# Optimization experiments

Hardware: AMD Instinct MI355X
Metric: run time of the kernel (lower is better)

The kernel has to match this reference:

```python
import jax, jax.numpy as jnp
import numpy as np

D = 256          # common_dim = specific_dim
NH = 8           # num_heads
HD = D // NH     # head_dim = 32
B, S = 16, 1024
EPS = 1e-5


def _mha(q, k, v, wq, bq, wk, bk, wv, bv, wo, bo):
    # q,k,v: [B, S, D]; weights stored [in, out] so y = x @ w + b
    b_, _, _ = q.shape

    def proj(x, w, b):
        return (x @ w + b).reshape(b_, -1, NH, HD).transpose(0, 2, 1, 3)  # [B,H,S,hd]

    Q, K, V = proj(q, wq, bq), proj(k, wk, bk), proj(v, wv, bv)
    scores = jnp.einsum('bhqd,bhkd->bhqk', Q, K) / (float(HD) ** 0.5)
    attn = jax.nn.softmax(scores, axis=-1)
    out = jnp.einsum('bhqk,bhkd->bhqd', attn, V)
    out = out.transpose(0, 2, 1, 3).reshape(b_, -1, D)
    return out @ wo + bo


def _ln(x, g, b):
    mu = jnp.mean(x, axis=-1, keepdims=True)
    var = jnp.var(x, axis=-1, keepdims=True)
    return (x - mu) * jax.lax.rsqrt(var + EPS) * g + b


def setup_inputs() -> dict:
    key = jax.random.key(0)
    ks = iter(jax.random.split(key, 32))
    rn = lambda *shape: jax.random.normal(next(ks), shape, dtype=jnp.float32)
    w = lambda i, o: rn(i, o) * 0.05
    inp = {
        'img_common': rn(B, S, D),
        'txt_common': rn(B, S, D),
        'img_specific': rn(B, D),
        'txt_specific': rn(B, D),
    }
    for pfx in ('i2t', 't2i'):
        for nm in ('q', 'k', 'v', 'o'):
            inp[f'{pfx}_w{nm}'] = w(D, D)
            inp[f'{pfx}_b{nm}'] = jnp.zeros((D,), jnp.float32)
    inp['ln_img_g'] = jnp.ones((D,), jnp.float32)
    inp['ln_img_b'] = jnp.zeros((D,), jnp.float32)
    inp['ln_txt_g'] = jnp.ones((D,), jnp.float32)
    inp['ln_txt_b'] = jnp.zeros((D,), jnp.float32)
    inp['enh_w'] = w(2 * D, D)
    inp['enh_b'] = jnp.zeros((D,), jnp.float32)
    inp['inc_w'] = w(2 * D, D)
    inp['inc_b'] = jnp.zeros((D,), jnp.float32)
    return inp


def reference(img_common, txt_common, img_specific, txt_specific,
              i2t_wq, i2t_bq, i2t_wk, i2t_bk, i2t_wv, i2t_bv, i2t_wo, i2t_bo,
              t2i_wq, t2i_bq, t2i_wk, t2i_bk, t2i_wv, t2i_bv, t2i_wo, t2i_bo,
              ln_img_g, ln_img_b, ln_txt_g, ln_txt_b,
              enh_w, enh_b, inc_w, inc_b):
    att_i2t = _mha(img_common, txt_common, txt_common,
                   i2t_wq, i2t_bq, i2t_wk, i2t_bk, i2t_wv, i2t_bv, i2t_wo, i2t_bo)
    img_query = _ln(att_i2t + img_common, ln_img_g, ln_img_b)
    att_t2i = _mha(txt_common, img_common, img_common,
                   t2i_wq, t2i_bq, t2i_wk, t2i_bk, t2i_wv, t2i_bv, t2i_wo, t2i_bo)
    txt_query = _ln(att_t2i + txt_common, ln_txt_g, ln_txt_b)
    combined = jnp.concatenate((img_query, txt_query), axis=-1)  # [B,S,2D]
    enhancement = combined @ enh_w + enh_b                        # [B,S,D]
    inc = jnp.concatenate((img_specific - txt_specific,
                           img_specific * txt_specific), axis=1)  # [B,2D]
    inconsistency = inc @ inc_w + inc_b                           # [B,D]
    return (enhancement, inconsistency, img_specific, txt_specific)
```

## Files before the change

kernel.cpp:

```cpp
#include <hip/hip_runtime.h>
#include <stdint.h>

typedef unsigned int u32;
typedef unsigned short u16;
typedef __attribute__((ext_vector_type(8))) short bf16x8;
typedef __attribute__((ext_vector_type(4))) float f32x4;

#define BUF_ELEMS (16384 * 256)

__device__ __forceinline__ float bflo(u32 u) { return __uint_as_float(u << 16); }
__device__ __forceinline__ float bfhi(u32 u) { return __uint_as_float(u & 0xffff0000u); }
__device__ __forceinline__ u16 f2bf(float f) {
    u32 u = __float_as_uint(f);
    return (u16)((u + 0x7fffu + ((u >> 16) & 1u)) >> 16);
}
__device__ __forceinline__ u32 pkhi(float lo, float hi) {
    return __builtin_amdgcn_perm(__float_as_uint(hi), __float_as_uint(lo), 0x07060302u);
}

struct WT {
    const float* src[9];
    u16* dst[9];
    const float* bs[6];
    float* bA;
    float* bB;
    const float* img_sp;
    const float* txt_sp;
    const float* incw;
    const float* incb;
    float* out_inc;
    float* out_img;
    float* out_txt;
};

__global__ __launch_bounds__(256)
void wtrans_kernel(WT wt)
{
    __shared__ float T[64][65];
    const int bid = blockIdx.x, t = threadIdx.x;
    if (bid == 160) {
        wt.bA[t]       = wt.bs[0][t];
        wt.bA[256 + t] = wt.bs[1][t];
        wt.bA[512 + t] = wt.bs[2][t];
        wt.bB[t]       = wt.bs[3][t];
        wt.bB[256 + t] = wt.bs[4][t];
        wt.bB[512 + t] = wt.bs[5][t];
        return;
    }
    if (bid > 160) {
        float* iv = &T[0][0];
        const int b = bid - 161, n = t;
        float a = wt.img_sp[b * 256 + n];
        float x = wt.txt_sp[b * 256 + n];
        iv[n] = a - x;
        iv[256 + n] = a * x;
        __syncthreads();
        float acc = wt.incb[n];
        for (int k = 0; k < 512; k++) acc += iv[k] * wt.incw[k * 256 + n];
        wt.out_inc[b * 256 + n] = acc;
        wt.out_img[b * 256 + n] = a;
        wt.out_txt[b * 256 + n] = x;
        return;
    }
    int m, sub;
    if (bid < 128) { m = bid >> 4; sub = bid & 15; }
    else           { m = 8;        sub = bid - 128; }
    const int K = (m == 8) ? 512 : 256;
    const int kt = (m == 8) ? (sub & 7) : (sub & 3);
    const int nt = (m == 8) ? (sub >> 3) : (sub >> 2);
    const int k0 = kt * 64, n0 = nt * 64;
    const float* src = wt.src[m];
    u16* dst = wt.dst[m];

    const int kk = t >> 2, nn = (t & 3) * 16;
    #pragma unroll
    for (int j = 0; j < 16; j += 4) {
        float4 v = *(const float4*)(src + (size_t)(k0 + kk) * 256 + n0 + nn + j);
        T[kk][nn + j + 0] = v.x; T[kk][nn + j + 1] = v.y;
        T[kk][nn + j + 2] = v.z; T[kk][nn + j + 3] = v.w;
    }
    __syncthreads();
    const int nn2 = t >> 2, kc = (t & 3) * 16;
    #pragma unroll
    for (int j = 0; j < 16; j++)
        dst[(size_t)(n0 + nn2) * K + k0 + kc + j] = f2bf(T[kc + j][nn2]);
}

template<int MODE>
__global__ __launch_bounds__(256)
void gemm_mfma(const float* __restrict__ Af0, const float* __restrict__ Af1,
               const u16* __restrict__ Ab0, const u16* __restrict__ Ab1,
               const u16* __restrict__ Wt0, const u16* __restrict__ Wt1,
               const float* __restrict__ bias0, const float* __restrict__ bias1,
               void* __restrict__ o0, void* __restrict__ o1, void* __restrict__ o2,
               void* __restrict__ o3, void* __restrict__ o4, void* __restrict__ o5)
{
    __shared__ u16 As[128][72];
    __shared__ u16 Bs[128][72];
    const int tid = threadIdx.x;
    const int wave = tid >> 6, lane = tid & 63;
    const int L = lane & 15, Qd = lane >> 4;
    int m_idx, n_idx;
    if (MODE == 0)      { m_idx = blockIdx.x & 255; n_idx = blockIdx.x >> 8; }
    else if (MODE == 1) { m_idx = blockIdx.x & 255; n_idx = blockIdx.x >> 8; }
    else                { m_idx = blockIdx.x & 127; n_idx = blockIdx.x >> 7; }
    const bool msel = (MODE != 2) && (m_idx >= 128 * (MODE == 0 ? 1 : 1) && MODE == 0
                       ? (m_idx >= 128) : (MODE == 1 && m_idx >= 128));
    const bool ms = (MODE == 0 || MODE == 1) ? (m_idx >= 128) : false;
    const int lm0 = (MODE == 2) ? m_idx * 128 : (m_idx & 127) * 128;
    const int n0 = n_idx * 128;
    const u16* Wt = ms ? Wt1 : Wt0;
    const float* bias = ms ? bias1 : bias0;
    const int wr = wave & 1, wc = wave >> 1;
    const int sr = tid >> 1, sh = (tid & 1) * 32;
    const int KS = (MODE == 2) ? 512 : 256;
    (void)msel;

    f32x4 acc[4][4] = {};

    for (int kt = 0; kt < KS; kt += 64) {
        if (MODE == 0) {
            const float* Af = ms ? Af1 : Af0;
            const float* Ap = Af + (size_t)(lm0 + sr) * 256 + kt + sh;
            uint4 pk[2];
            #pragma unroll
            for (int half = 0; half < 2; half++) {
                float4 f0 = *(const float4*)(Ap + half * 16);
                float4 f1 = *(const float4*)(Ap + half * 16 + 4);
                float4 f2 = *(const float4*)(Ap + half * 16 + 8);
                float4 f3 = *(const float4*)(Ap + half * 16 + 12);
                pk[half].x = pkhi(f0.x, f0.y);
                pk[half].y = pkhi(f0.z, f0.w);
                pk[half].z = pkhi(f1.x, f1.y);
                pk[half].w = pkhi(f1.z, f1.w);
                uint4 q;
                q.x = pkhi(f2.x, f2.y); q.y = pkhi(f2.z, f2.w);
                q.z = pkhi(f3.x, f3.y); q.w = pkhi(f3.z, f3.w);
                *(uint4*)&As[sr][sh + half * 16 + 8] = q;
            }
            *(uint4*)&As[sr][sh + 0] = pk[0];
            *(uint4*)&As[sr][sh + 16] = pk[1];
        } else {
            const u16* Abase;
            int lkt = kt;
            if (MODE == 2) { Abase = (kt < 256) ? Ab0 : Ab1; lkt = kt & 255; }
            else           { Abase = ms ? Ab1 : Ab0; }
            const u16* Ap = Abase + (size_t)(lm0 + sr) * 256 + lkt + sh;
            uint4 a0 = *(const uint4*)(Ap + 0);
            uint4 a1 = *(const uint4*)(Ap + 8);
            uint4 a2 = *(const uint4*)(Ap + 16);
            uint4 a3 = *(const uint4*)(Ap + 24);
            *(uint4*)&As[sr][sh + 0]  = a0;
            *(uint4*)&As[sr][sh + 8]  = a1;
            *(uint4*)&As[sr][sh + 16] = a2;
            *(uint4*)&As[sr][sh + 24] = a3;
        }
        {
            const u16* Bp = Wt + (size_t)(n0 + sr) * KS + kt + sh;
            uint4 w0 = *(const uint4*)(Bp + 0);
            uint4 w1 = *(const uint4*)(Bp + 8);
            uint4 w2 = *(const uint4*)(Bp + 16);
            uint4 w3 = *(const uint4*)(Bp + 24);
            *(uint4*)&Bs[sr][sh + 0]  = w0;
            *(uint4*)&Bs[sr][sh + 8]  = w1;
            *(uint4*)&Bs[sr][sh + 16] = w2;
            *(uint4*)&Bs[sr][sh + 24] = w3;
        }
        __syncthreads();
        #pragma unroll
        for (int kh = 0; kh < 64; kh += 32) {
            bf16x8 af[4], bf[4];
            #pragma unroll
            for (int mt = 0; mt < 4; mt++)
                af[mt] = *(const bf16x8*)&As[wr * 64 + mt * 16 + L][kh + Qd * 8];
            #pragma unroll
            for (int nt = 0; nt < 4; nt++)
                bf[nt] = *(const bf16x8*)&Bs[wc * 64 + nt * 16 + L][kh + Qd * 8];
            #pragma unroll
            for (int mt = 0; mt < 4; mt++)
                #pragma unroll
                for (int nt = 0; nt < 4; nt++)
                    acc[mt][nt] = __builtin_amdgcn_mfma_f32_16x16x32_bf16(
                        af[mt], bf[nt], acc[mt][nt], 0, 0, 0);
        }
        __syncthreads();
    }

    float bvals[4];
    #pragma unroll
    for (int nt = 0; nt < 4; nt++)
        bvals[nt] = bias[n0 + wc * 64 + nt * 16 + L];

    const float qsc = (MODE == 0 && n_idx < 2)
                      ? (0.17677669529663687f * 1.4426950408889634f) : 1.0f;

    void* outp;
    int colb;
    if (MODE == 0) {
        const int g = n_idx >> 1;
        if (!ms) outp = (g == 0) ? o0 : ((g == 1) ? o1 : o2);
        else     outp = (g == 0) ? o3 : ((g == 1) ? o4 : o5);
        colb = (n_idx & 1) * 128 + wc * 64;
    } else if (MODE == 1) {
        outp = ms ? o1 : o0;
        colb = n0 + wc * 64;
    } else {
        outp = o0;
        colb = n0 + wc * 64;
    }
    #pragma unroll
    for (int mt = 0; mt < 4; mt++) {
        #pragma unroll
        for (int r = 0; r < 4; r++) {
            const size_t row = (size_t)(lm0 + wr * 64 + mt * 16 + Qd * 4 + r) * 256;
            #pragma unroll
            for (int nt = 0; nt < 4; nt++) {
                const int col = colb + nt * 16 + L;
                float v = (acc[mt][nt][r] + bvals[nt]) * qsc;
                if (MODE == 2) ((float*)outp)[row + col] = v;
                else           ((u16*)outp)[row + col] = f2bf(v);
            }
        }
    }
}

__global__ __launch_bounds__(256, 4)
void attn_mfma(const u16* __restrict__ Q0, const u16* __restrict__ K0,
               const u16* __restrict__ V0, u16* __restrict__ O0,
               const u16* __restrict__ Q1, const u16* __restrict__ K1,
               const u16* __restrict__ V1, u16* __restrict__ O1)
{
    __shared__ u16 Ks[128][40];
    __shared__ u16 Vt[32][136];
    __shared__ u16 Ps[4][16][136];
    const int tid = threadIdx.x;
    const int wave = tid >> 6, lane = tid & 63;
    const int L = lane & 15, Qd = lane >> 4;
    const int bid = blockIdx.x;
    const int qt = bid >> 8;
    const int kv = bid & 255;
    const int set = kv >> 7;
    const int b = (kv >> 3) & 15;
    const int h = kv & 7;
    const u16* Q = set ? Q1 : Q0;
    const u16* K = set ? K1 : K0;
    const u16* V = set ? V1 : V0;
    u16* O = set ? O1 : O0;
    const int rowbase = b * 1024;
    const int qbase = rowbase + qt * 128;

    bf16x8 qfrag[2];
    #pragma unroll
    for (int qs = 0; qs < 2; qs++)
        qfrag[qs] = *(const bf16x8*)(Q + (size_t)(qbase + qs * 64 + wave * 16 + L) * 256
                                       + h * 32 + Qd * 8);

    const short oneb = (short)0x3F80;
    const bf16x8 ones = {oneb, oneb, oneb, oneb, oneb, oneb, oneb, oneb};

    f32x4 oacc[2][2] = {};
    f32x4 oaccL[2] = {};

    const int sr = tid >> 1;
    const int scol = (tid & 1) * 16;
    const int vcol = (sr & 15) * 8 + (sr >> 4);

    for (int t = 0; t < 8; t++) {
        const size_t kvbase = (size_t)(rowbase + t * 128 + sr) * 256 + h * 32 + scol;
        uint4 k1 = *(const uint4*)(K + kvbase);
        uint4 k2 = *(const uint4*)(K + kvbase + 8);
        uint4 v1 = *(const uint4*)(V + kvbase);
        uint4 v2 = *(const uint4*)(V + kvbase + 8);
        *(uint4*)&Ks[sr][scol]     = k1;
        *(uint4*)&Ks[sr][scol + 8] = k2;
        union { uint4 u4[2]; u16 us[16]; } vv;
        vv.u4[0] = v1; vv.u4[1] = v2;
        #pragma unroll
        for (int j = 0; j < 16; j++) Vt[scol + j][vcol] = vv.us[j];
        __syncthreads();

        bf16x8 kf[8];
        #pragma unroll
        for (int ct = 0; ct < 8; ct++)
            kf[ct] = *(const bf16x8*)&Ks[ct * 16 + L][Qd * 8];

        #pragma unroll
        for (int qs = 0; qs < 2; qs++) {
            const f32x4 z = {0.f, 0.f, 0.f, 0.f};
            f32x4 sacc[8];
            #pragma unroll
            for (int ct = 0; ct < 8; ct++)
                sacc[ct] = __builtin_amdgcn_mfma_f32_16x16x32_bf16(qfrag[qs], kf[ct], z, 0, 0, 0);
            #pragma unroll
            for (int r = 0; r < 4; r++) {
                float p[8];
                #pragma unroll
                for (int ct = 0; ct < 8; ct++) p[ct] = exp2f(sacc[ct][r]);
                uint4 pk;
                pk.x = pkhi(p[0], p[1]);
                pk.y = pkhi(p[2], p[3]);
                pk.z = pkhi(p[4], p[5]);
                pk.w = pkhi(p[6], p[7]);
                *(uint4*)&Ps[wave][Qd * 4 + r][L * 8] = pk;
            }
            #pragma unroll
            for (int kc = 0; kc < 4; kc++) {
                bf16x8 pfrag = *(const bf16x8*)&Ps[wave][L][kc * 32 + Qd * 8];
                bf16x8 vf0 = *(const bf16x8*)&Vt[L][kc * 32 + Qd * 8];
                bf16x8 vf1 = *(const bf16x8*)&Vt[16 + L][kc * 32 + Qd * 8];
                oacc[qs][0] = __builtin_amdgcn_mfma_f32_16x16x32_bf16(pfrag, vf0, oacc[qs][0], 0, 0, 0);
                oacc[qs][1] = __builtin_amdgcn_mfma_f32_16x16x32_bf16(pfrag, vf1, oacc[qs][1], 0, 0, 0);
                oaccL[qs]   = __builtin_amdgcn_mfma_f32_16x16x32_bf16(pfrag, ones, oaccL[qs], 0, 0, 0);
            }
        }
        __syncthreads();
    }

    #pragma unroll
    for (int qs = 0; qs < 2; qs++) {
        #pragma unroll
        for (int r = 0; r < 4; r++) {
            float inv = 1.f / oaccL[qs][r];
            const size_t orow = (size_t)(qbase + qs * 64 + wave * 16 + Qd * 4 + r) * 256 + h * 32;
            O[orow + L]      = f2bf(oacc[qs][0][r] * inv);
            O[orow + 16 + L] = f2bf(oacc[qs][1][r] * inv);
        }
    }
}

__global__ __launch_bounds__(256)
void ln_res_kernel(const u16* __restrict__ P0, const u16* __restrict__ P1,
                   const float* __restrict__ R0, const float* __restrict__ R1,
                   const float* __restrict__ g0, const float* __restrict__ be0,
                   const float* __restrict__ g1, const float* __restrict__ be1,
                   u16* __restrict__ out0, u16* __restrict__ out1)
{
    const int lane = threadIdx.x & 63;
    int row = blockIdx.x * 4 + (threadIdx.x >> 6);
    const bool sel = row >= 16384;
    const u16* P = sel ? P1 : P0;
    const float* R = sel ? R1 : R0;
    const float* g = sel ? g1 : g0;
    const float* be = sel ? be1 : be0;
    u16* out = sel ? out1 : out0;
    if (sel) row -= 16384;
    const int col = lane * 4;
    uint2 pv = *(const uint2*)(P + (size_t)row * 256 + col);
    float4 rv = *(const float4*)(R + (size_t)row * 256 + col);
    float x0 = bflo(pv.x) + rv.x;
    float x1 = bfhi(pv.x) + rv.y;
    float x2 = bflo(pv.y) + rv.z;
    float x3 = bfhi(pv.y) + rv.w;
    float s = x0 + x1 + x2 + x3;
    float s2 = x0*x0 + x1*x1 + x2*x2 + x3*x3;
    #pragma unroll
    for (int off = 32; off > 0; off >>= 1) {
        s  += __shfl_xor(s, off);
        s2 += __shfl_xor(s2, off);
    }
    float mean = s * 0.00390625f;
    float var = fmaxf(s2 * 0.00390625f - mean * mean, 0.f);
    float rstd = rsqrtf(var + 1e-5f);
    float4 gv = *(const float4*)(g + col);
    float4 bv = *(const float4*)(be + col);
    uint2 pk;
    pk.x = (u32)f2bf((x0 - mean) * rstd * gv.x + bv.x)
         | ((u32)f2bf((x1 - mean) * rstd * gv.y + bv.y) << 16);
    pk.y = (u32)f2bf((x2 - mean) * rstd * gv.z + bv.z)
         | ((u32)f2bf((x3 - mean) * rstd * gv.w + bv.w) << 16);
    *(uint2*)(out + (size_t)row * 256 + col) = pk;
}

extern "C" void kernel_launch(void* const* d_in, const int* in_sizes, int n_in,
                              void* d_out, int out_size, void* d_ws, size_t ws_size,
                              hipStream_t stream)
{
    (void)in_sizes; (void)n_in; (void)out_size; (void)ws_size;
    const float* img    = (const float*)d_in[0];
    const float* txt    = (const float*)d_in[1];
    const float* img_sp = (const float*)d_in[2];
    const float* txt_sp = (const float*)d_in[3];
    const float* wq_i = (const float*)d_in[4];  const float* bq_i = (const float*)d_in[5];
    const float* wk_i = (const float*)d_in[6];  const float* bk_i = (const float*)d_in[7];
    const float* wv_i = (const float*)d_in[8];  const float* bv_i = (const float*)d_in[9];
    const float* wo_i = (const float*)d_in[10]; const float* bo_i = (const float*)d_in[11];
    const float* wq_t = (const float*)d_in[12]; const float* bq_t = (const float*)d_in[13];
    const float* wk_t = (const float*)d_in[14]; const float* bk_t = (const float*)d_in[15];
    const float* wv_t = (const float*)d_in[16]; const float* bv_t = (const float*)d_in[17];
    const float* wo_t = (const float*)d_in[18]; const float* bo_t = (const float*)d_in[19];
    const float* lng_i = (const float*)d_in[20]; const float* lnb_i = (const float*)d_in[21];
    const float* lng_t = (const float*)d_in[22]; const float* lnb_t = (const float*)d_in[23];
    const float* enh_w = (const float*)d_in[24]; const float* enh_b = (const float*)d_in[25];
    const float* incw  = (const float*)d_in[26]; const float* incb  = (const float*)d_in[27];
    float* out = (float*)d_out;
    u16* wsp = (u16*)d_ws;
    u16* B0 = wsp;
    u16* B1 = wsp + 1 * (size_t)BUF_ELEMS;
    u16* B2 = wsp + 2 * (size_t)BUF_ELEMS;
    u16* B3 = wsp + 3 * (size_t)BUF_ELEMS;
    u16* B4 = wsp + 4 * (size_t)BUF_ELEMS;
    u16* B5 = wsp + 5 * (size_t)BUF_ELEMS;
    u16* wbase = wsp + 6 * (size_t)BUF_ELEMS;
    u16* WtA   = wbase;
    u16* WtB   = wbase + 196608;
    u16* Wt_oi = wbase + 393216;
    u16* Wt_ot = wbase + 458752;
    u16* Wt_en = wbase + 524288;
    float* biasA = (float*)(wbase + 655360);
    float* biasB = biasA + 768;

    dim3 blk(256);
    WT wt;
    wt.src[0] = wq_i; wt.dst[0] = WtA;
    wt.src[1] = wk_t; wt.dst[1] = WtA + 65536;
    wt.src[2] = wv_t; wt.dst[2] = WtA + 131072;
    wt.src[3] = wq_t; wt.dst[3] = WtB;
    wt.src[4] = wk_i; wt.dst[4] = WtB + 65536;
    wt.src[5] = wv_i; wt.dst[5] = WtB + 131072;
    wt.src[6] = wo_i; wt.dst[6] = Wt_oi;
    wt.src[7] = wo_t; wt.dst[7] = Wt_ot;
    wt.src[8] = enh_w; wt.dst[8] = Wt_en;
    wt.bs[0] = bq_i; wt.bs[1] = bk_t; wt.bs[2] = bv_t;
    wt.bs[3] = bq_t; wt.bs[4] = bk_i; wt.bs[5] = bv_i;
    wt.bA = biasA; wt.bB = biasB;
    wt.img_sp = img_sp; wt.txt_sp = txt_sp; wt.incw = incw; wt.incb = incb;
    wt.out_inc = out + 4194304; wt.out_img = out + 4198400; wt.out_txt = out + 4202496;
    wtrans_kernel<<<177, blk, 0, stream>>>(wt);

    gemm_mfma<0><<<1536, blk, 0, stream>>>(img, txt, nullptr, nullptr,
                                           WtA, WtB, biasA, biasB,
                                           B0, B4, B5, B3, B1, B2);
    attn_mfma<<<2048, blk, 0, stream>>>(B0, B1, B2, B0, B3, B4, B5, B3);
    gemm_mfma<1><<<512, blk, 0, stream>>>(nullptr, nullptr, B0, B3,
                                          Wt_oi, Wt_ot, bo_i, bo_t,
                                          B1, B4, nullptr, nullptr, nullptr, nullptr);
    ln_res_kernel<<<8192, blk, 0, stream>>>(B1, B4, img, txt,
                                            lng_i, lnb_i, lng_t, lnb_t, B2, B5);
    gemm_mfma<2><<<256, blk, 0, stream>>>(nullptr, nullptr, B2, B5,
                                          Wt_en, nullptr, enh_b, nullptr,
                                          out, nullptr, nullptr, nullptr, nullptr, nullptr);
}
```

Before: 309.8 us.

## Swizzle block order for L2 reuse, load K fragments directly, move inconsistency GEMV

Block indices in the projection GEMMs and the attention kernel are remapped into groups of eight so that neighbouring blocks share weight or K/V tiles in cache. The attention kernel drops the K staging through LDS and loads K fragments straight from global memory, which frees LDS and raises the occupancy hint from 4 to 5. The small inconsistency GEMV and the pass-through copies move from the weight-transpose kernel into extra blocks of the final GEMM launch. Each K element is now read from global by several lanes instead of once through LDS, so more memory traffic is traded for less LDS use and fewer barriers.

```diff
diff --git a/kernel.cpp b/kernel.cpp
--- a/kernel.cpp
+++ b/kernel.cpp
@@ -24,13 +24,6 @@
     const float* bs[6];
     float* bA;
     float* bB;
-    const float* img_sp;
-    const float* txt_sp;
-    const float* incw;
-    const float* incb;
-    float* out_inc;
-    float* out_img;
-    float* out_txt;
 };
 
 __global__ __launch_bounds__(256)
@@ -47,21 +40,6 @@
         wt.bB[512 + t] = wt.bs[5][t];
         return;
     }
-    if (bid > 160) {
-        float* iv = &T[0][0];
-        const int b = bid - 161, n = t;
-        float a = wt.img_sp[b * 256 + n];
-        float x = wt.txt_sp[b * 256 + n];
-        iv[n] = a - x;
-        iv[256 + n] = a * x;
-        __syncthreads();
-        float acc = wt.incb[n];
-        for (int k = 0; k < 512; k++) acc += iv[k] * wt.incw[k * 256 + n];
-        wt.out_inc[b * 256 + n] = acc;
-        wt.out_img[b * 256 + n] = a;
-        wt.out_txt[b * 256 + n] = x;
-        return;
-    }
     int m, sub;
     if (bid < 128) { m = bid >> 4; sub = bid & 15; }
     else           { m = 8;        sub = bid - 128; }
@@ -98,15 +76,41 @@
     __shared__ u16 As[128][72];
     __shared__ u16 Bs[128][72];
     const int tid = threadIdx.x;
+
+    if (MODE == 2 && blockIdx.x >= 256) {
+        float* iv = (float*)&As[0][0];
+        const int b = blockIdx.x - 256, n = tid;
+        float a = Af0[b * 256 + n];
+        float x = Af1[b * 256 + n];
+        iv[n] = a - x;
+        iv[256 + n] = a * x;
+        __syncthreads();
+        const float* Wi = (const float*)Wt1;
+        float a0 = bias1[n], a1 = 0.f, a2 = 0.f, a3 = 0.f;
+        #pragma unroll 2
+        for (int k = 0; k < 512; k += 4) {
+            a0 += iv[k]     * Wi[(k)     * 256 + n];
+            a1 += iv[k + 1] * Wi[(k + 1) * 256 + n];
+            a2 += iv[k + 2] * Wi[(k + 2) * 256 + n];
+            a3 += iv[k + 3] * Wi[(k + 3) * 256 + n];
+        }
+        ((float*)o1)[b * 256 + n] = (a0 + a1) + (a2 + a3);
+        ((float*)o2)[b * 256 + n] = a;
+        ((float*)o3)[b * 256 + n] = x;
+        return;
+    }
+
     const int wave = tid >> 6, lane = tid & 63;
     const int L = lane & 15, Qd = lane >> 4;
     int m_idx, n_idx;
-    if (MODE == 0)      { m_idx = blockIdx.x & 255; n_idx = blockIdx.x >> 8; }
-    else if (MODE == 1) { m_idx = blockIdx.x & 255; n_idx = blockIdx.x >> 8; }
-    else                { m_idx = blockIdx.x & 127; n_idx = blockIdx.x >> 7; }
-    const bool msel = (MODE != 2) && (m_idx >= 128 * (MODE == 0 ? 1 : 1) && MODE == 0
-                       ? (m_idx >= 128) : (MODE == 1 && m_idx >= 128));
-    const bool ms = (MODE == 0 || MODE == 1) ? (m_idx >= 128) : false;
+    if (MODE == 0) {
+        const int sup = blockIdx.x / 48, rem = blockIdx.x % 48;
+        n_idx = rem >> 3; m_idx = sup * 8 + (rem & 7);
+    } else {
+        const int sup = blockIdx.x >> 4, rem = blockIdx.x & 15;
+        n_idx = (rem >> 3) & 1; m_idx = sup * 8 + (rem & 7);
+    }
+    const bool ms = (MODE != 2) && (m_idx >= 128);
     const int lm0 = (MODE == 2) ? m_idx * 128 : (m_idx & 127) * 128;
     const int n0 = n_idx * 128;
     const u16* Wt = ms ? Wt1 : Wt0;
@@ -114,7 +118,6 @@
     const int wr = wave & 1, wc = wave >> 1;
     const int sr = tid >> 1, sh = (tid & 1) * 32;
     const int KS = (MODE == 2) ? 512 : 256;
-    (void)msel;
 
     f32x4 acc[4][4] = {};
 
@@ -224,24 +227,24 @@
     }
 }
 
-__global__ __launch_bounds__(256, 4)
+__global__ __launch_bounds__(256, 5)
 void attn_mfma(const u16* __restrict__ Q0, const u16* __restrict__ K0,
                const u16* __restrict__ V0, u16* __restrict__ O0,
                const u16* __restrict__ Q1, const u16* __restrict__ K1,
                const u16* __restrict__ V1, u16* __restrict__ O1)
 {
-    __shared__ u16 Ks[128][40];
     __shared__ u16 Vt[32][136];
     __shared__ u16 Ps[4][16][136];
     const int tid = threadIdx.x;
     const int wave = tid >> 6, lane = tid & 63;
     const int L = lane & 15, Qd = lane >> 4;
     const int bid = blockIdx.x;
-    const int qt = bid >> 8;
-    const int kv = bid & 255;
-    const int set = kv >> 7;
-    const int b = (kv >> 3) & 15;
-    const int h = kv & 7;
+    const int sup = bid >> 6, rem = bid & 63;
+    const int qt = rem >> 3;
+    const int kvl = sup * 8 + (rem & 7);
+    const int set = kvl >> 7;
+    const int b = (kvl >> 3) & 15;
+    const int h = kvl & 7;
     const u16* Q = set ? Q1 : Q0;
     const u16* K = set ? K1 : K0;
     const u16* V = set ? V1 : V0;
@@ -267,22 +270,20 @@
 
     for (int t = 0; t < 8; t++) {
         const size_t kvbase = (size_t)(rowbase + t * 128 + sr) * 256 + h * 32 + scol;
-        uint4 k1 = *(const uint4*)(K + kvbase);
-        uint4 k2 = *(const uint4*)(K + kvbase + 8);
         uint4 v1 = *(const uint4*)(V + kvbase);
         uint4 v2 = *(const uint4*)(V + kvbase + 8);
-        *(uint4*)&Ks[sr][scol]     = k1;
-        *(uint4*)&Ks[sr][scol + 8] = k2;
         union { uint4 u4[2]; u16 us[16]; } vv;
         vv.u4[0] = v1; vv.u4[1] = v2;
         #pragma unroll
         for (int j = 0; j < 16; j++) Vt[scol + j][vcol] = vv.us[j];
+
+        const u16* Kb = K + (size_t)(rowbase + t * 128 + L) * 256 + h * 32 + Qd * 8;
+        bf16x8 kf[8];
+        #pragma unroll
+        for (int ct = 0; ct < 8; ct++)
+            kf[ct] = *(const bf16x8*)(Kb + (size_t)ct * 16 * 256);
+
         __syncthreads();
-
-        bf16x8 kf[8];
-        #pragma unroll
-        for (int ct = 0; ct < 8; ct++)
-            kf[ct] = *(const bf16x8*)&Ks[ct * 16 + L][Qd * 8];
 
         #pragma unroll
         for (int qs = 0; qs < 2; qs++) {
@@ -423,9 +424,7 @@
     wt.bs[0] = bq_i; wt.bs[1] = bk_t; wt.bs[2] = bv_t;
     wt.bs[3] = bq_t; wt.bs[4] = bk_i; wt.bs[5] = bv_i;
     wt.bA = biasA; wt.bB = biasB;
-    wt.img_sp = img_sp; wt.txt_sp = txt_sp; wt.incw = incw; wt.incb = incb;
-    wt.out_inc = out + 4194304; wt.out_img = out + 4198400; wt.out_txt = out + 4202496;
-    wtrans_kernel<<<177, blk, 0, stream>>>(wt);
+    wtrans_kernel<<<161, blk, 0, stream>>>(wt);
 
     gemm_mfma<0><<<1536, blk, 0, stream>>>(img, txt, nullptr, nullptr,
                                            WtA, WtB, biasA, biasB,
@@ -436,7 +435,8 @@
                                           B1, B4, nullptr, nullptr, nullptr, nullptr);
     ln_res_kernel<<<8192, blk, 0, stream>>>(B1, B4, img, txt,
                                             lng_i, lnb_i, lng_t, lnb_t, B2, B5);
-    gemm_mfma<2><<<256, blk, 0, stream>>>(nullptr, nullptr, B2, B5,
-                                          Wt_en, nullptr, enh_b, nullptr,
-                                          out, nullptr, nullptr, nullptr, nullptr, nullptr);
-}
+    gemm_mfma<2><<<272, blk, 0, stream>>>(img_sp, txt_sp, B2, B5,
+                                          Wt_en, (const u16*)incw, enh_b, incb,
+                                          out, out + 4194304, out + 4198400,
+                                          out + 4202496, nullptr, nullptr);
+}
```

After: 369.5 us. +19.3%, slower.
